# Kernel tuning notes

Measured on AMD Instinct MI355X. Metric: run time of the kernel, lower is better.

## Reference

```python
import jax, jax.numpy as jnp
import numpy as np

NUM_HEADS = 16


def setup_inputs() -> dict:
    key = jax.random.key(0)
    ks = jax.random.split(key, 9)
    B, S, C = 2, 2048, 1024
    s = 1.0 / np.sqrt(C)
    return {
        "hidden_states": jax.random.normal(ks[0], (B, S, C), jnp.float32),
        "Wq": jax.random.normal(ks[1], (C, C), jnp.float32) * s,
        "bq": jnp.zeros((C,), jnp.float32),
        "Wk": jax.random.normal(ks[2], (C, C), jnp.float32) * s,
        "bk": jnp.zeros((C,), jnp.float32),
        "Wv": jax.random.normal(ks[3], (C, C), jnp.float32) * s,
        "bv": jnp.zeros((C,), jnp.float32),
        "Wo": jax.random.normal(ks[4], (C, C), jnp.float32) * s,
        "bo": jnp.zeros((C,), jnp.float32),
    }


def reference(hidden_states, Wq, bq, Wk, bk, Wv, bv, Wo, bo):
    # Self-attention path of AttnProcessor (3D input, no mask, no norms,
    # residual_connection=True, rescale_output_factor=1.0).
    B, S, C = hidden_states.shape
    H = NUM_HEADS
    D = C // H
    residual = hidden_states

    q = hidden_states @ Wq + bq  # [B,S,C]
    k = hidden_states @ Wk + bk
    v = hidden_states @ Wv + bv

    # head_to_batch_dim: [B,S,C] -> [B,S,H,D]
    q = q.reshape(B, S, H, D)
    k = k.reshape(B, S, H, D)
    v = v.reshape(B, S, H, D)

    scale = 1.0 / np.sqrt(D).astype(np.float32)
    # get_attention_scores: baddbmm with scale, then softmax (full [B,H,S,S])
    scores = jnp.einsum("bqhd,bkhd->bhqk", q, k) * scale
    probs = jax.nn.softmax(scores, axis=-1)

    out = jnp.einsum("bhqk,bkhd->bqhd", probs, v)  # bmm(probs, value)
    out = out.reshape(B, S, C)  # batch_to_head_dim

    out = out @ Wo + bo  # to_out[0]; to_out[1] is dropout (identity in eval)
    out = out + residual  # residual_connection
    return out  # rescale_output_factor = 1.0
```

## Files before the change

### kernel.cpp

```cpp
#include <hip/hip_runtime.h>

#define BATCH 2
#define SEQ   2048
#define CH    1024
#define NHEAD 16
#define HDIM  64
#define MROWS (BATCH * SEQ)

typedef __attribute__((ext_vector_type(8))) short short8;
typedef __attribute__((ext_vector_type(4))) float floatx4;
typedef unsigned short ushort_t;

__device__ __forceinline__ float b2f(ushort_t u) {
    union { unsigned int i; float f; } x;
    x.i = ((unsigned int)u) << 16;
    return x.f;
}
__device__ __forceinline__ ushort_t f2b(float f) {
    union { float f; unsigned int i; } x;
    x.f = f;
    unsigned int lsb = (x.i >> 16) & 1u;
    x.i += 0x7fffu + lsb;
    return (ushort_t)(x.i >> 16);
}
__device__ __forceinline__ unsigned pack2(float a, float b) {
    return (unsigned)f2b(a) | ((unsigned)f2b(b) << 16);
}
__device__ __forceinline__ unsigned cvt_pk_bf16(float a, float b) {
    unsigned r;
    asm("v_cvt_pk_bf16_f32 %0, %1, %2" : "=v"(r) : "v"(a), "v"(b));
    return r;
}

__device__ __forceinline__ void gld16(const ushort_t* g, ushort_t* l) {
    __builtin_amdgcn_global_load_lds(
        (const __attribute__((address_space(1))) void*)g,
        (__attribute__((address_space(3))) void*)l, 16, 0, 0);
}

template <int VM>
__device__ __forceinline__ void vm_barrier() {
    asm volatile("s_waitcnt vmcnt(%0) lgkmcnt(0)\n\ts_barrier" ::"i"(VM)
                 : "memory");
}

__global__ __launch_bounds__(256) void cvt_bf16_kernel(
    const float* __restrict__ in, ushort_t* __restrict__ out, int n4) {
    int i = blockIdx.x * blockDim.x + threadIdx.x;
    if (i < n4) {
        float4 v = ((const float4*)in)[i];
        ushort4 o = {f2b(v.x), f2b(v.y), f2b(v.z), f2b(v.w)};
        ((ushort4*)out)[i] = o;
    }
}

__global__ __launch_bounds__(256) void transpose_cvt_all(
    const float* __restrict__ W0, const float* __restrict__ W1,
    const float* __restrict__ W2, const float* __restrict__ W3,
    ushort_t* __restrict__ T0, ushort_t* __restrict__ T1,
    ushort_t* __restrict__ T2, ushort_t* __restrict__ T3) {
    __shared__ ushort_t T[64][68];
    const int z = blockIdx.z;
    const float* W = (z == 0) ? W0 : (z == 1) ? W1 : (z == 2) ? W2 : W3;
    ushort_t* Wt = (z == 0) ? T0 : (z == 1) ? T1 : (z == 2) ? T2 : T3;
    const int tid = threadIdx.x;
    const int n0 = blockIdx.x * 64, k0 = blockIdx.y * 64;
    const int r = tid >> 4, c4 = (tid & 15) * 4;
#pragma unroll
    for (int p = 0; p < 4; p++) {
        int k = p * 16 + r;
        float4 v = *(const float4*)&W[(size_t)(k0 + k) * CH + n0 + c4];
        T[c4 + 0][k] = f2b(v.x);
        T[c4 + 1][k] = f2b(v.y);
        T[c4 + 2][k] = f2b(v.z);
        T[c4 + 3][k] = f2b(v.w);
    }
    __syncthreads();
#pragma unroll
    for (int p = 0; p < 4; p++) {
        int n = p * 16 + r;
        ushort4 o = {T[n][c4 + 0], T[n][c4 + 1], T[n][c4 + 2], T[n][c4 + 3]};
        *(ushort4*)&Wt[(size_t)(n0 + n) * CH + k0 + c4] = o;
    }
}

__device__ __forceinline__ void gemm_core_db(
    const ushort_t* __restrict__ A, const ushort_t* __restrict__ Bt,
    int bm, int n0, int tid, floatx4 acc[4][4], ushort_t* lds) {
    const int wave = tid >> 6, lane = tid & 63;
    const int quad = lane >> 4, t16 = lane & 15;
    const int wm = wave >> 1, wn = wave & 1;
    const int arow = tid >> 2, ak = (tid & 3) * 8;

    const ushort_t* a0 = A + (size_t)(bm + arow) * CH + ak;
    const ushort_t* a1 = A + (size_t)(bm + 64 + arow) * CH + ak;
    const ushort_t* b0 = Bt + (size_t)(n0 + arow) * CH + ak;
    const ushort_t* b1 = Bt + (size_t)(n0 + 64 + arow) * CH + ak;

#pragma unroll
    for (int i = 0; i < 4; i++)
#pragma unroll
        for (int j = 0; j < 4; j++) acc[i][j] = (floatx4){0.f, 0.f, 0.f, 0.f};

    auto stage = [&](int k, ushort_t* buf) {
        gld16(a0 + k, buf + wave * 512);
        gld16(a1 + k, buf + 2048 + wave * 512);
        gld16(b0 + k, buf + 4096 + wave * 512);
        gld16(b1 + k, buf + 6144 + wave * 512);
    };
    auto compute = [&](const ushort_t* As) {
        const ushort_t* Bs = As + 4096;
        short8 af[4], bf[4];
#pragma unroll
        for (int i = 0; i < 4; i++)
            af[i] = *(const short8*)&As[(wm * 64 + i * 16 + t16) * 32 + quad * 8];
#pragma unroll
        for (int j = 0; j < 4; j++)
            bf[j] = *(const short8*)&Bs[(wn * 64 + j * 16 + t16) * 32 + quad * 8];
#pragma unroll
        for (int i = 0; i < 4; i++)
#pragma unroll
            for (int j = 0; j < 4; j++)
                acc[i][j] = __builtin_amdgcn_mfma_f32_16x16x32_bf16(
                    af[i], bf[j], acc[i][j], 0, 0, 0);
    };

    ushort_t* bcur = lds;
    ushort_t* bnext = lds + 8192;
    ushort_t* bfar = lds + 16384;

    stage(0, bcur);
    stage(32, bnext);

    for (int it = 0; it < CH / 32 - 2; ++it) {
        vm_barrier<4>();
        stage((it + 2) * 32, bfar);
        compute(bcur);
        ushort_t* t = bcur; bcur = bnext; bnext = bfar; bfar = t;
    }
    vm_barrier<4>();
    compute(bcur);
    vm_barrier<0>();
    compute(bnext);
}

__global__ __launch_bounds__(256) void gemm_qkv(
    const ushort_t* __restrict__ X,
    const ushort_t* __restrict__ WqT, const ushort_t* __restrict__ WkT,
    const ushort_t* __restrict__ WvT,
    const float* __restrict__ bq, const float* __restrict__ bk,
    const float* __restrict__ bv,
    ushort_t* __restrict__ Qm, ushort_t* __restrict__ Km,
    ushort_t* __restrict__ Vtm) {
    __shared__ ushort_t lds[3 * 8192];
    const int tid = threadIdx.x;
    const int seg = blockIdx.x >> 3;
    const int n0 = (blockIdx.x & 7) * 128;
    const int bm = blockIdx.y * 128;
    const ushort_t* Bt = (seg == 0) ? WqT : (seg == 1) ? WkT : WvT;
    const float* bias = (seg == 0) ? bq : (seg == 1) ? bk : bv;

    floatx4 acc[4][4];
    gemm_core_db(X, Bt, bm, n0, tid, acc, lds);

    const int lane = tid & 63, wave = tid >> 6;
    const int quad = lane >> 4, t16 = lane & 15;
    const int wm = wave >> 1, wn = wave & 1;

    if (seg < 2) {
        ushort_t* outp = seg ? Km : Qm;
        const float sc = seg ? 1.0f : 0.125f;
#pragma unroll
        for (int i = 0; i < 4; i++)
#pragma unroll
            for (int j = 0; j < 4; j++) {
                const int col = n0 + wn * 64 + j * 16 + t16;
                const float bb = bias[col];
                const int row0 = bm + wm * 64 + i * 16 + quad * 4;
#pragma unroll
                for (int r = 0; r < 4; r++)
                    outp[(size_t)(row0 + r) * CH + col] =
                        f2b((acc[i][j][r] + bb) * sc);
            }
    } else {
        ushort_t* rep = lds;
        const int b = bm >> 11;
        const int s_base = bm & (SEQ - 1);
#pragma unroll
        for (int half = 0; half < 2; half++) {
            __syncthreads();
            if (wn == half) {
#pragma unroll
                for (int i = 0; i < 4; i++)
#pragma unroll
                    for (int j = 0; j < 4; j++) {
                        const int dl = j * 16 + t16;
                        const int sl = wm * 64 + i * 16 + quad * 4;
                        const float bb = bias[n0 + half * 64 + dl];
                        uint2 w = {pack2(acc[i][j][0] + bb, acc[i][j][1] + bb),
                                   pack2(acc[i][j][2] + bb, acc[i][j][3] + bb)};
                        *(uint2*)&rep[dl * 136 + sl] = w;
                    }
            }
            __syncthreads();
#pragma unroll
            for (int step = 0; step < 4; step++) {
                const int dl = step * 16 + (tid >> 4);
                const int sl = (tid & 15) * 8;
                short8 v = *(const short8*)&rep[dl * 136 + sl];
                const int col = n0 + half * 64 + dl;
                const int h = col >> 6, dd = col & 63;
                *(short8*)&Vtm[(((size_t)b * NHEAD + h) * HDIM + dd) * SEQ +
                               s_base + sl] = v;
            }
        }
    }
}

__global__ __launch_bounds__(256) void gemm_out(
    const ushort_t* __restrict__ Am, const ushort_t* __restrict__ WoT,
    const float* __restrict__ bo, const float* __restrict__ resid,
    float* __restrict__ out) {
    __shared__ ushort_t lds[3 * 6144];
    const int tid = threadIdx.x;
    const int n0 = blockIdx.x * 64;
    const int bm = blockIdx.y * 128;
    const int wave = tid >> 6, lane = tid & 63;
    const int quad = lane >> 4, t16 = lane & 15;
    const int arow = tid >> 2, ak = (tid & 3) * 8;

    const ushort_t* a0 = Am + (size_t)(bm + arow) * CH + ak;
    const ushort_t* a1 = Am + (size_t)(bm + 64 + arow) * CH + ak;
    const ushort_t* b0 = WoT + (size_t)(n0 + arow) * CH + ak;

    floatx4 acc[2][4];
#pragma unroll
    for (int i = 0; i < 2; i++)
#pragma unroll
        for (int j = 0; j < 4; j++) acc[i][j] = (floatx4){0.f, 0.f, 0.f, 0.f};

    auto stage = [&](int k, ushort_t* buf) {
        gld16(a0 + k, buf + wave * 512);
        gld16(a1 + k, buf + 2048 + wave * 512);
        gld16(b0 + k, buf + 4096 + wave * 512);
    };
    auto compute = [&](const ushort_t* As) {
        const ushort_t* Bs = As + 4096;
        short8 af[2], bf[4];
#pragma unroll
        for (int i = 0; i < 2; i++)
            af[i] = *(const short8*)&As[(wave * 32 + i * 16 + t16) * 32 + quad * 8];
#pragma unroll
        for (int j = 0; j < 4; j++)
            bf[j] = *(const short8*)&Bs[(j * 16 + t16) * 32 + quad * 8];
#pragma unroll
        for (int i = 0; i < 2; i++)
#pragma unroll
            for (int j = 0; j < 4; j++)
                acc[i][j] = __builtin_amdgcn_mfma_f32_16x16x32_bf16(
                    af[i], bf[j], acc[i][j], 0, 0, 0);
    };

    ushort_t* bcur = lds;
    ushort_t* bnext = lds + 6144;
    ushort_t* bfar = lds + 12288;

    stage(0, bcur);
    stage(32, bnext);

    for (int it = 0; it < CH / 32 - 2; ++it) {
        vm_barrier<3>();
        stage((it + 2) * 32, bfar);
        compute(bcur);
        ushort_t* t = bcur; bcur = bnext; bnext = bfar; bfar = t;
    }
    vm_barrier<3>();
    compute(bcur);
    vm_barrier<0>();
    compute(bnext);

#pragma unroll
    for (int i = 0; i < 2; i++)
#pragma unroll
        for (int j = 0; j < 4; j++) {
            const int col = n0 + j * 16 + t16;
            const float bb = bo[col];
            const int row0 = bm + wave * 32 + i * 16 + quad * 4;
#pragma unroll
            for (int r = 0; r < 4; r++) {
                const size_t idx = (size_t)(row0 + r) * CH + col;
                out[idx] = acc[i][j][r] + bb + resid[idx];
            }
        }
}

__global__ __launch_bounds__(512, 4) void flash_attn_mfma(
    const ushort_t* __restrict__ Q, const ushort_t* __restrict__ K,
    const ushort_t* __restrict__ Vt, ushort_t* __restrict__ O) {
    __shared__ ushort_t Ks[64][72];
    __shared__ ushort_t Vs[64][72];

    const int tid = threadIdx.x;
    const int wave = tid >> 6, lane = tid & 63;
    const int quad = lane >> 4, t16 = lane & 15;
    const int bh = blockIdx.y, b = bh >> 4, h = bh & 15;
    const int q0 = blockIdx.x * 128;

    const size_t base_q = ((size_t)b * SEQ) * CH + (size_t)h * HDIM;
    const size_t base_vt = ((size_t)(b * NHEAD + h)) * HDIM * SEQ;

    short8 qf[2];
    {
        const ushort_t* qp =
            Q + base_q + (size_t)(q0 + wave * 16 + t16) * CH + quad * 8;
        qf[0] = *(const short8*)(qp);
        qf[1] = *(const short8*)(qp + 32);
    }

    const short8 ones = (short8)(short)0x3F80;

    floatx4 Oa[4];
    floatx4 Oe = (floatx4){0.f, 0.f, 0.f, 0.f};
#pragma unroll
    for (int d = 0; d < 4; d++) Oa[d] = (floatx4){0.f, 0.f, 0.f, 0.f};

    const int r4 = tid >> 3;
    const int t8 = tid & 7;
    const int c8 = t8 * 8;
    const ushort_t* kp = K + base_q + (size_t)r4 * CH + c8;
    const ushort_t* vp = Vt + base_vt + (size_t)r4 * SEQ + c8;

    const int vcol0 = ((t8 & 4) << 3) + (((2 * t8) & 3) << 3) + (((t8 >> 1) & 1) << 2);
    const int vcol1 = ((t8 & 4) << 3) + (((2 * t8 + 1) & 3) << 3) + (((t8 >> 1) & 1) << 2);

    short8 kreg = *(const short8*)(kp);
    short8 vreg = *(const short8*)(vp);

    for (int k0 = 0; k0 < SEQ; k0 += 64) {
        __syncthreads();
        *(short8*)&Ks[r4][c8] = kreg;
        {
            union { short8 s; uint4 u; } vv; vv.s = vreg;
            *(uint2*)&Vs[r4][vcol0] = (uint2){vv.u.x, vv.u.y};
            *(uint2*)&Vs[r4][vcol1] = (uint2){vv.u.z, vv.u.w};
        }
        __syncthreads();
        if (k0 + 64 < SEQ) {
            kreg = *(const short8*)(kp + (size_t)(k0 + 64) * CH);
            vreg = *(const short8*)(vp + (k0 + 64));
        }

        uint2 pw[4];
#pragma unroll
        for (int j = 0; j < 4; j++) {
            short8 kf0 = *(const short8*)(&Ks[j * 16 + t16][quad * 8]);
            short8 kf1 = *(const short8*)(&Ks[j * 16 + t16][32 + quad * 8]);
            floatx4 z = (floatx4){0.f, 0.f, 0.f, 0.f};
            z = __builtin_amdgcn_mfma_f32_16x16x32_bf16(kf0, qf[0], z, 0, 0, 0);
            z = __builtin_amdgcn_mfma_f32_16x16x32_bf16(kf1, qf[1], z, 0, 0, 0);
            pw[j].x = cvt_pk_bf16(__expf(z[0]), __expf(z[1]));
            pw[j].y = cvt_pk_bf16(__expf(z[2]), __expf(z[3]));
        }
        short8 pf0, pf1;
        {
            union { uint4 u; short8 s; } c0, c1;
            c0.u = (uint4){pw[0].x, pw[0].y, pw[1].x, pw[1].y};
            c1.u = (uint4){pw[2].x, pw[2].y, pw[3].x, pw[3].y};
            pf0 = c0.s;
            pf1 = c1.s;
        }

        __builtin_amdgcn_s_setprio(1);
#pragma unroll
        for (int d = 0; d < 4; d++) {
            short8 vf0 = *(const short8*)(&Vs[d * 16 + t16][quad * 8]);
            short8 vf1 = *(const short8*)(&Vs[d * 16 + t16][32 + quad * 8]);
            Oa[d] = __builtin_amdgcn_mfma_f32_16x16x32_bf16(pf0, vf0, Oa[d], 0, 0, 0);
            Oa[d] = __builtin_amdgcn_mfma_f32_16x16x32_bf16(pf1, vf1, Oa[d], 0, 0, 0);
        }
        Oe = __builtin_amdgcn_mfma_f32_16x16x32_bf16(pf0, ones, Oe, 0, 0, 0);
        Oe = __builtin_amdgcn_mfma_f32_16x16x32_bf16(pf1, ones, Oe, 0, 0, 0);
        __builtin_amdgcn_s_setprio(0);
    }

    float inv[4];
#pragma unroll
    for (int r = 0; r < 4; r++) inv[r] = 1.f / Oe[r];
#pragma unroll
    for (int d = 0; d < 4; d++)
#pragma unroll
        for (int r = 0; r < 4; r++) {
            const int row = q0 + wave * 16 + quad * 4 + r;
            O[base_q + (size_t)row * CH + d * 16 + t16] =
                f2b(Oa[d][r] * inv[r]);
        }
}

extern "C" void kernel_launch(void* const* d_in, const int* in_sizes, int n_in,
                              void* d_out, int out_size, void* d_ws,
                              size_t ws_size, hipStream_t stream) {
    const float* X  = (const float*)d_in[0];
    const float* Wq = (const float*)d_in[1];
    const float* bq = (const float*)d_in[2];
    const float* Wk = (const float*)d_in[3];
    const float* bk = (const float*)d_in[4];
    const float* Wv = (const float*)d_in[5];
    const float* bv = (const float*)d_in[6];
    const float* Wo = (const float*)d_in[7];
    const float* bo = (const float*)d_in[8];
    float* out = (float*)d_out;

    const size_t MC = (size_t)MROWS * CH;
    const size_t WC = (size_t)CH * CH;
    ushort_t* ws  = (ushort_t*)d_ws;
    ushort_t* X16 = ws;
    ushort_t* Am  = ws;
    ushort_t* Qm  = ws + MC;
    ushort_t* Km  = ws + 2 * MC;
    ushort_t* Vtm = ws + 3 * MC;
    ushort_t* WqT = ws + 4 * MC;
    ushort_t* WkT = ws + 4 * MC + WC;
    ushort_t* WvT = ws + 4 * MC + 2 * WC;
    ushort_t* WoT = ws + 4 * MC + 3 * WC;

    dim3 blk(256);

    cvt_bf16_kernel<<<dim3((MC / 4 + 255) / 256), blk, 0, stream>>>(X, X16, (int)(MC / 4));
    transpose_cvt_all<<<dim3(16, 16, 4), blk, 0, stream>>>(
        Wq, Wk, Wv, Wo, WqT, WkT, WvT, WoT);

    gemm_qkv<<<dim3(24, 32), blk, 0, stream>>>(X16, WqT, WkT, WvT, bq, bk, bv,
                                               Qm, Km, Vtm);

    flash_attn_mfma<<<dim3(SEQ / 128, BATCH * NHEAD), dim3(512), 0, stream>>>(
        Qm, Km, Vtm, Am);

    gemm_out<<<dim3(16, 32), blk, 0, stream>>>(Am, WoT, bo, X, out);
}
```

Measured before the change: 188.9 us.

## Double-buffer flash attention K/V via direct global-to-LDS loads with XOR swizzle

```diff
diff --git a/kernel.cpp b/kernel.cpp
--- a/kernel.cpp
+++ b/kernel.cpp
@@ -210,8 +210,18 @@
                 short8 v = *(const short8*)&rep[dl * 136 + sl];
                 const int col = n0 + half * 64 + dl;
                 const int h = col >> 6, dd = col & 63;
-                *(short8*)&Vtm[(((size_t)b * NHEAD + h) * HDIM + dd) * SEQ +
-                               s_base + sl] = v;
+                const int c = (sl >> 3) & 7;
+                const int r7 = dd & 7;
+                const int slot0 = (c & 4) | ((2 * c) & 3);
+                const int slot1 = (c & 4) | ((2 * c + 1) & 3);
+                const int sub = ((c >> 1) & 1) << 2;
+                ushort_t* vrow = Vtm +
+                    (((size_t)b * NHEAD + h) * HDIM + dd) * SEQ + s_base +
+                    (sl & 64);
+                union { short8 s; uint2 u[2]; } vv;
+                vv.s = v;
+                *(uint2*)&vrow[((slot0 ^ r7) << 3) + sub] = vv.u[0];
+                *(uint2*)&vrow[((slot1 ^ r7) << 3) + sub] = vv.u[1];
             }
         }
     }
@@ -297,8 +307,7 @@
 __global__ __launch_bounds__(512, 4) void flash_attn_mfma(
     const ushort_t* __restrict__ Q, const ushort_t* __restrict__ K,
     const ushort_t* __restrict__ Vt, ushort_t* __restrict__ O) {
-    __shared__ ushort_t Ks[64][72];
-    __shared__ ushort_t Vs[64][72];
+    __shared__ __attribute__((aligned(16))) ushort_t smem[2][2][64][64];
 
     const int tid = threadIdx.x;
     const int wave = tid >> 6, lane = tid & 63;
@@ -324,37 +333,32 @@
 #pragma unroll
     for (int d = 0; d < 4; d++) Oa[d] = (floatx4){0.f, 0.f, 0.f, 0.f};
 
-    const int r4 = tid >> 3;
-    const int t8 = tid & 7;
-    const int c8 = t8 * 8;
-    const ushort_t* kp = K + base_q + (size_t)r4 * CH + c8;
-    const ushort_t* vp = Vt + base_vt + (size_t)r4 * SEQ + c8;
-
-    const int vcol0 = ((t8 & 4) << 3) + (((2 * t8) & 3) << 3) + (((t8 >> 1) & 1) << 2);
-    const int vcol1 = ((t8 & 4) << 3) + (((2 * t8 + 1) & 3) << 3) + (((t8 >> 1) & 1) << 2);
-
-    short8 kreg = *(const short8*)(kp);
-    short8 vreg = *(const short8*)(vp);
-
-    for (int k0 = 0; k0 < SEQ; k0 += 64) {
-        __syncthreads();
-        *(short8*)&Ks[r4][c8] = kreg;
-        {
-            union { short8 s; uint4 u; } vv; vv.s = vreg;
-            *(uint2*)&Vs[r4][vcol0] = (uint2){vv.u.x, vv.u.y};
-            *(uint2*)&Vs[r4][vcol1] = (uint2){vv.u.z, vv.u.w};
-        }
-        __syncthreads();
-        if (k0 + 64 < SEQ) {
-            kreg = *(const short8*)(kp + (size_t)(k0 + 64) * CH);
-            vreg = *(const short8*)(vp + (k0 + 64));
-        }
+    const int sr = tid >> 3;
+    const int ss = tid & 7;
+    const ushort_t* ksrc = K + base_q + (size_t)sr * CH + ((ss ^ (sr & 7)) << 3);
+    const ushort_t* vsrc = Vt + base_vt + (size_t)sr * SEQ + (ss << 3);
+
+    auto stage = [&](int k0, int buf) {
+        gld16(ksrc + (size_t)k0 * CH, &smem[buf][0][0][0] + wave * 512);
+        gld16(vsrc + k0, &smem[buf][1][0][0] + wave * 512);
+    };
+
+    const int koff0 = (quad ^ (t16 & 7)) << 3;
+    const int koff1 = ((quad + 4) ^ (t16 & 7)) << 3;
+
+    stage(0, 0);
+
+    for (int t = 0; t < SEQ / 64; ++t) {
+        vm_barrier<0>();
+        if (t + 1 < SEQ / 64) stage((t + 1) * 64, (t + 1) & 1);
+        const ushort_t* Kb = &smem[t & 1][0][0][0];
+        const ushort_t* Vb = &smem[t & 1][1][0][0];
 
         uint2 pw[4];
 #pragma unroll
         for (int j = 0; j < 4; j++) {
-            short8 kf0 = *(const short8*)(&Ks[j * 16 + t16][quad * 8]);
-            short8 kf1 = *(const short8*)(&Ks[j * 16 + t16][32 + quad * 8]);
+            short8 kf0 = *(const short8*)&Kb[(j * 16 + t16) * 64 + koff0];
+            short8 kf1 = *(const short8*)&Kb[(j * 16 + t16) * 64 + koff1];
             floatx4 z = (floatx4){0.f, 0.f, 0.f, 0.f};
             z = __builtin_amdgcn_mfma_f32_16x16x32_bf16(kf0, qf[0], z, 0, 0, 0);
             z = __builtin_amdgcn_mfma_f32_16x16x32_bf16(kf1, qf[1], z, 0, 0, 0);
@@ -373,8 +377,8 @@
         __builtin_amdgcn_s_setprio(1);
 #pragma unroll
         for (int d = 0; d < 4; d++) {
-            short8 vf0 = *(const short8*)(&Vs[d * 16 + t16][quad * 8]);
-            short8 vf1 = *(const short8*)(&Vs[d * 16 + t16][32 + quad * 8]);
+            short8 vf0 = *(const short8*)&Vb[(d * 16 + t16) * 64 + koff0];
+            short8 vf1 = *(const short8*)&Vb[(d * 16 + t16) * 64 + koff1];
             Oa[d] = __builtin_amdgcn_mfma_f32_16x16x32_bf16(pf0, vf0, Oa[d], 0, 0, 0);
             Oa[d] = __builtin_amdgcn_mfma_f32_16x16x32_bf16(pf1, vf1, Oa[d], 0, 0, 0);
         }
```

New measurement: 189.1 us, median of 2. Within noise of the previous version (+0.1%).
